# Kernel tuning notes

Measured on AMD Instinct MI355X. Metric: run time of the kernel, lower is better.

## Reference

```python
import jax, jax.numpy as jnp
import numpy as np

OBS_LEN, PRED_LEN, N, NUM_SEQ = 8, 12, 512, 8
H_ENC, H_DEC, EMB, NOISE_DIM = 8, 16, 16, 8


def setup_inputs() -> dict:
    key = jax.random.key(0)
    ks = jax.random.split(key, 32)
    def rn(i, shape, std=1.0):
        return jax.random.normal(ks[i], shape, jnp.float32) * std
    bounds = np.arange(NUM_SEQ + 1) * (N // NUM_SEQ)
    bih_t = jnp.zeros(4 * H_ENC, jnp.float32).at[H_ENC:2 * H_ENC].set(1.0)  # forget bias 1
    bih_p = jnp.zeros(4 * H_DEC, jnp.float32).at[H_DEC:2 * H_DEC].set(1.0)
    return {
        'traj_rel': rn(0, (OBS_LEN + PRED_LEN, N, 2)),
        'obs_traj_pos': rn(1, (OBS_LEN, N, 2), 5.0),
        'pred_traj_gt_pos': rn(2, (PRED_LEN, N, 2), 5.0),
        'h0': rn(3, (N, H_ENC)), 'c0': rn(4, (N, H_ENC)),
        'noise': rn(5, (NUM_SEQ, NOISE_DIM)),
        'W_enc': rn(6, (EMB, 2), 0.2), 'b_enc': jnp.zeros(EMB, jnp.float32),
        'W_dec': rn(7, (EMB, H_DEC + 2), 0.2), 'b_dec': jnp.zeros(EMB, jnp.float32),
        'Wih_t': rn(8, (4 * H_ENC, EMB), 0.1), 'Whh_t': rn(9, (4 * H_ENC, H_ENC), 0.001),
        'bih_t': bih_t, 'bhh_t': jnp.zeros(4 * H_ENC, jnp.float32),
        'Wih_p': rn(10, (4 * H_DEC, EMB), 0.1), 'Whh_p': rn(11, (4 * H_DEC, H_DEC), 0.001),
        'bih_p': bih_p, 'bhh_p': jnp.zeros(4 * H_DEC, jnp.float32),
        'W_out': rn(12, (2, H_DEC), 0.1), 'b_out': jnp.zeros(2, jnp.float32),
        'W_se': rn(13, (EMB, 2), 0.1), 'b_se': jnp.zeros(EMB, jnp.float32),
        'W_m1': rn(14, (64, EMB + H_DEC), 0.1), 'b_m1': jnp.zeros(64, jnp.float32),
        'W_m2': rn(15, (H_DEC, 64), 0.1), 'b_m2': jnp.zeros(H_DEC, jnp.float32),
        'W_att': rn(16, (1, H_DEC), 0.1), 'b_att': jnp.zeros(1, jnp.float32),
        'seq_start_end': jnp.asarray(np.stack([bounds[:-1], bounds[1:]], 1), jnp.int32),
        'nei_index': jax.random.randint(ks[17], (PRED_LEN, N, N), 0, 2, jnp.int32),
        'nei_num_index': jnp.full((N,), N // 2, jnp.int32),
    }


def _lstm_cell(x, h, c, Wih, Whh, bih, bhh):
    g = x @ Wih.T + bih + h @ Whh.T + bhh
    i, f, gg, o = jnp.split(g, 4, axis=-1)
    c2 = jax.nn.sigmoid(f) * c + jax.nn.sigmoid(i) * jnp.tanh(gg)
    return jax.nn.sigmoid(o) * jnp.tanh(c2), c2


def reference(traj_rel, obs_traj_pos, pred_traj_gt_pos, h0, c0, noise,
              W_enc, b_enc, W_dec, b_dec,
              Wih_t, Whh_t, bih_t, bhh_t,
              Wih_p, Whh_p, bih_p, bhh_p,
              W_out, b_out, W_se, b_se, W_m1, b_m1, W_m2, b_m2, W_att, b_att,
              seq_start_end, nei_index, nei_num_index):
    nb = traj_rel.shape[1]

    # ---- encoder: obs_len tiny LSTM steps over relative displacements ----
    def enc_step(carry, x_t):
        h, c = carry
        e = jax.nn.relu(x_t @ W_enc.T + b_enc)
        h, c = _lstm_cell(e, h, c, Wih_t, Whh_t, bih_t, bhh_t)
        return (h, c), None
    (h_enc, _), _ = jax.lax.scan(enc_step, (h0, c0), traj_rel[:OBS_LEN])

    # ---- add global per-scene noise (noise_mix_type == 'global') ----
    seq_ids = jnp.searchsorted(seq_start_end[:, 0], jnp.arange(nb), side='right') - 1
    dec_h = jnp.concatenate([h_enc, noise[seq_ids]], axis=1)  # [N, 16]

    def pool(pos, mask, h):
        # corr_index[i,j] = pos[i] - pos[j]
        corr = pos[:, None, :] - pos[None, :, :]                 # [N,N,2]
        r = corr @ W_se.T + b_se                                 # [N,N,EMB]
        hj = jnp.broadcast_to(h[None, :, :], (nb, nb, H_DEC))    # neighbor hidden
        m_in = jnp.concatenate([r, hj], axis=-1)                 # [N,N,EMB+H]
        h1 = jax.nn.relu(m_in @ W_m1.T + b_m1)                   # [N,N,64]
        pre = jax.nn.relu(h1 @ W_m2.T + b_m2)                    # [N,N,H]
        s = jnp.squeeze(pre @ W_att.T + b_att, -1)               # [N,N]
        s = jnp.where(mask, s, -1e9)
        w = jax.nn.softmax(s, axis=-1)
        ctx = jnp.einsum('ij,ijh->ih', w, pre)
        return jnp.where(mask.any(-1, keepdims=True), ctx, 0.0)

    # ---- decoder: pred_len steps with social pooling each step ----
    sg = jax.lax.stop_gradient
    init = (dec_h, jnp.zeros_like(dec_h), jnp.zeros_like(dec_h),
            jnp.zeros((nb, 2), dec_h.dtype), obs_traj_pos[-1])

    def dec_step(carry, nei_t):
        h, c, ctx, out, pos = carry
        inp_cat = jnp.concatenate([sg(ctx), sg(out)], axis=-1)   # [N, 18]
        e = jax.nn.relu(inp_cat @ W_dec.T + b_dec)
        h, c = _lstm_cell(e, h, c, Wih_p, Whh_p, bih_p, bhh_p)
        ctx = pool(pos, nei_t > 0, h)
        out = jnp.tanh((ctx + h) @ W_out.T + b_out) * 4.4
        pos = sg(pos + out)
        return (h, c, ctx, out, pos), out

    _, pred_traj_rel = jax.lax.scan(dec_step, init, nei_index)
    return pred_traj_rel  # [pred_len, N, 2]
```

## Files before the change

kernel.cpp:

```cpp
#include <hip/hip_runtime.h>
#include <math.h>

#define NPED 512
#define OBS 8
#define PRED 12
#define HE 8
#define HD 16
#define EMB 16
#define NZ 8
#define NSEQ 8

typedef const float* fp;
typedef float f4 __attribute__((ext_vector_type(4)));

__device__ __forceinline__ float frcp(float x){ return __builtin_amdgcn_rcpf(x); }
__device__ __forceinline__ float sigm(float x){ return frcp(1.0f + __expf(-x)); }
__device__ __forceinline__ float tanh_f(float x){ return 1.0f - 2.0f*frcp(__expf(2.0f*x) + 1.0f); }

#define WS_H    0
#define WS_C    (WS_H + NPED*HD)
#define WS_POS0 (WS_C + NPED*HD)
#define WS_POS1 (WS_POS0 + NPED*2)
#define WS_HB0  (WS_POS1 + NPED*2)
#define WS_HB1  (WS_HB0 + NPED*64)
#define WS_A0   (WS_HB1 + NPED*64)
#define WS_A1   (WS_A0 + 64)
#define WS_BB   (WS_A1 + 64)
#define WS_WM2T (WS_BB + 64)

__global__ __launch_bounds__(256) void init_kernel(
        fp traj, fp obs_pos, fp h0, fp c0, fp noise,
        fp Wenc, fp benc, fp Wih, fp Whh, fp bih, fp bhh,
        fp bdec, fp Wihp, fp Whhp, fp bihp, fp bhhp, fp Wm1,
        fp Wse, fp bse, fp bm1, fp Wm2,
        const int* sse, float* ws)
{
    __shared__ float s_wenc[32], s_benc[16], s_wihT[32*17], s_whhT[32*9], s_bT[32];
    __shared__ float s_wihP[64*17], s_whhP[64*17], s_wm1h[64*17], s_bP[64], s_e0[16];
    __shared__ float s_hc[16*16];
    int tid = threadIdx.x;

    if (blockIdx.x == 0) {
        if (tid < 64) {
            float a0 = 0.f, a1 = 0.f, bb = bm1[tid];
            for (int kk = 0; kk < 16; kk++) {
                float w = Wm1[tid*32 + kk];
                a0 += w*Wse[kk*2+0]; a1 += w*Wse[kk*2+1]; bb += w*bse[kk];
            }
            ws[WS_A0 + tid] = a0; ws[WS_A1 + tid] = a1; ws[WS_BB + tid] = bb;
        }
        for (int i = tid; i < 1024; i += 256) {
            int u = i >> 4, v = i & 15;
            ws[WS_WM2T + u*16 + v] = Wm2[v*64 + u];
        }
    }

    if (tid < 32) { s_wenc[tid] = Wenc[tid]; s_bT[tid] = bih[tid] + bhh[tid]; }
    if (tid < 16) { s_benc[tid] = benc[tid]; s_e0[tid] = fmaxf(bdec[tid], 0.f); }
    for (int i = tid; i < 512; i += 256) s_wihT[(i>>4)*17 + (i&15)] = Wih[i];
    { int i = tid; if (i < 256) s_whhT[(i>>3)*9 + (i&7)] = Whh[i]; }
    for (int i = tid; i < 1024; i += 256) {
        int r = i>>4, d = i&15;
        s_wihP[r*17+d] = Wihp[i];
        s_whhP[r*17+d] = Whhp[i];
        s_wm1h[r*17+d] = Wm1[r*32 + 16 + d];
    }
    if (tid < 64) s_bP[tid] = bihp[tid] + bhhp[tid];
    __syncthreads();

    int pid = tid >> 4, k16 = tid & 15;
    int n = blockIdx.x*16 + pid;

    if (k16 < 8) {
        int k = k16;
        float h = h0[n*HE+k], c = c0[n*HE+k];
        for (int t = 0; t < OBS; t++) {
            float x0 = traj[(t*NPED+n)*2+0];
            float x1 = traj[(t*NPED+n)*2+1];
            float g0 = s_bT[k], g1 = s_bT[8+k], g2 = s_bT[16+k], g3 = s_bT[24+k];
            #pragma unroll
            for (int d = 0; d < EMB; d++) {
                float e = fmaxf(s_wenc[d*2]*x0 + s_wenc[d*2+1]*x1 + s_benc[d], 0.f);
                g0 += s_wihT[(k)*17+d]*e;    g1 += s_wihT[(8+k)*17+d]*e;
                g2 += s_wihT[(16+k)*17+d]*e; g3 += s_wihT[(24+k)*17+d]*e;
            }
            #pragma unroll
            for (int d = 0; d < HE; d++) {
                float hv = __shfl(h, d, 8);
                g0 += s_whhT[(k)*9+d]*hv;    g1 += s_whhT[(8+k)*9+d]*hv;
                g2 += s_whhT[(16+k)*9+d]*hv; g3 += s_whhT[(24+k)*9+d]*hv;
            }
            c = sigm(g1)*c + sigm(g0)*tanh_f(g2);
            h = sigm(g3)*tanh_f(c);
        }
        int cnt = 0;
        #pragma unroll
        for (int s2 = 0; s2 < NSEQ; s2++) cnt += (sse[s2*2] <= n) ? 1 : 0;
        s_hc[pid*16 + k]     = h;
        s_hc[pid*16 + 8 + k] = noise[(cnt-1)*NZ + k];
    }
    __syncthreads();

    int k = k16;
    float h = s_hc[pid*16 + k];
    float g0 = s_bP[k], g1 = s_bP[16+k], g2 = s_bP[32+k], g3 = s_bP[48+k];
    #pragma unroll
    for (int d = 0; d < HD; d++) {
        float ev = s_e0[d];
        float hv = __shfl(h, d, 16);
        g0 += s_wihP[(k)*17+d]*ev    + s_whhP[(k)*17+d]*hv;
        g1 += s_wihP[(16+k)*17+d]*ev + s_whhP[(16+k)*17+d]*hv;
        g2 += s_wihP[(32+k)*17+d]*ev + s_whhP[(32+k)*17+d]*hv;
        g3 += s_wihP[(48+k)*17+d]*ev + s_whhP[(48+k)*17+d]*hv;
    }
    float c = sigm(g0)*tanh_f(g2);
    float hn = sigm(g3)*tanh_f(c);
    ws[WS_H + n*HD + k] = hn;
    ws[WS_C + n*HD + k] = c;

    float hb0=0.f, hb1=0.f, hb2=0.f, hb3=0.f;
    #pragma unroll
    for (int d = 0; d < HD; d++) {
        float hv = __shfl(hn, d, 16);
        hb0 += s_wm1h[(k)*17+d]*hv;    hb1 += s_wm1h[(16+k)*17+d]*hv;
        hb2 += s_wm1h[(32+k)*17+d]*hv; hb3 += s_wm1h[(48+k)*17+d]*hv;
    }
    float* hb = ws + WS_HB0 + n*64;
    hb[k] = hb0; hb[16+k] = hb1; hb[32+k] = hb2; hb[48+k] = hb3;
    if (k < 2) ws[WS_POS0 + n*2 + k] = obs_pos[((OBS-1)*NPED+n)*2 + k];
}

__global__ __launch_bounds__(512, 4) void pool_step_kernel(
        int t, int last, const int* nei,
        fp Wm1, fp bm2, fp Watt, fp batt,
        fp Wdec, fp bdec, fp Wihp, fp Whhp, fp bihp, fp bhhp, fp Wout, fp bout,
        float* ws, float* dout)
{
    __shared__ __align__(16) float s_A0[64], s_A1[64], s_BB[64];
    __shared__ __align__(16) float s_wm2t[1024];
    __shared__ __align__(16) float s_bm2[16], s_watt[16];
    __shared__ float s_batt;
    __shared__ float s_posx[NPED], s_posy[NPED];
    __shared__ int   s_list[NPED], s_cnt[8];
    __shared__ float s_mat[16*512];
    __shared__ float s_lred[8], s_mred[8], s_ctxacc[16], s_ctx[16];
    __shared__ float s_wdec[16*19], s_bdec[16], s_wout[32], s_bout[2];
    int tid = threadIdx.x;
    int i = blockIdx.x;

    int a = nei[((size_t)t*NPED + i)*NPED + tid] > 0;

    if (tid < 64) { s_A0[tid] = ws[WS_A0+tid]; s_A1[tid] = ws[WS_A1+tid]; s_BB[tid] = ws[WS_BB+tid]; }
    if (tid < 256) ((float4*)s_wm2t)[tid] = ((const float4*)(ws + WS_WM2T))[tid];
    if (tid < 16) { s_bm2[tid] = bm2[tid]; s_watt[tid] = Watt[tid]; }
    if (tid == 0) s_batt = batt[0];
    for (int q = tid; q < 288; q += 512) s_wdec[(q/18)*19 + (q%18)] = Wdec[q];
    if (tid < 16) s_bdec[tid] = bdec[tid];
    if (tid < 32) s_wout[tid] = Wout[tid];
    if (tid < 2)  s_bout[tid] = bout[tid];

    const float* posrd = ws + ((t & 1) ? WS_POS1 : WS_POS0);
    const float* hbrd  = ws + ((t & 1) ? WS_HB1  : WS_HB0 );
    float* poswr = ws + ((t & 1) ? WS_POS0 : WS_POS1);
    float* hbwr  = ws + ((t & 1) ? WS_HB0  : WS_HB1 );
    {
        const float2* p2 = (const float2*)posrd;
        float2 pp = p2[tid];
        s_posx[tid] = pp.x; s_posy[tid] = pp.y;
    }

    int w = tid >> 6, lane = tid & 63;
    unsigned long long below = (1ull << lane) - 1ull;

    unsigned long long mb = __ballot(a);
    if (lane == 0) s_cnt[w] = __popcll(mb);
    __syncthreads();
    int cnt = 0, base = 0;
    #pragma unroll
    for (int q = 0; q < 8; q++) {
        int cq = s_cnt[q];
        cnt += cq;
        if (q < w) base += cq;
    }
    if (a) s_list[base + __popcll(mb & below)] = tid;
    __syncthreads();

    float pix = s_posx[i], piy = s_posy[i];
    f4 pre4[4];
    #pragma unroll
    for (int q = 0; q < 4; q++) pre4[q] = (f4){0.f,0.f,0.f,0.f};
    float sc = -INFINITY;

    if (tid < cnt) {
        const f4* bm24 = (const f4*)s_bm2;
        pre4[0] = bm24[0]; pre4[1] = bm24[1]; pre4[2] = bm24[2]; pre4[3] = bm24[3];
        int j = s_list[tid];
        float cx = pix - s_posx[j], cy = piy - s_posy[j];
        const f4* HB4 = (const f4*)(hbrd + j*64);
        const f4* A04 = (const f4*)s_A0;
        const f4* A14 = (const f4*)s_A1;
        const f4* BB4 = (const f4*)s_BB;
        #pragma unroll
        for (int uq = 0; uq < 16; uq++) {
            f4 hb = HB4[uq];
            f4 h14 = A04[uq]*cx + A14[uq]*cy + (BB4[uq] + hb);
            h14 = __builtin_elementwise_max(h14, (f4){0.f,0.f,0.f,0.f});
            #define ACCU(s_, hval_) { \
                f4 hs = (f4){hval_, hval_, hval_, hval_}; \
                const f4* wr = (const f4*)(s_wm2t + (uq*4 + s_)*16); \
                pre4[0] = __builtin_elementwise_fma(wr[0], hs, pre4[0]); \
                pre4[1] = __builtin_elementwise_fma(wr[1], hs, pre4[1]); \
                pre4[2] = __builtin_elementwise_fma(wr[2], hs, pre4[2]); \
                pre4[3] = __builtin_elementwise_fma(wr[3], hs, pre4[3]); }
            ACCU(0, h14.x) ACCU(1, h14.y) ACCU(2, h14.z) ACCU(3, h14.w)
            #undef ACCU
        }
        f4 sacc = (f4){0.f,0.f,0.f,0.f};
        const f4* wa4 = (const f4*)s_watt;
        #pragma unroll
        for (int q = 0; q < 4; q++) {
            pre4[q] = __builtin_elementwise_max(pre4[q], (f4){0.f,0.f,0.f,0.f});
            sacc = __builtin_elementwise_fma(pre4[q], wa4[q], sacc);
        }
        sc = s_batt + (sacc.x + sacc.y) + (sacc.z + sacc.w);
    }

    float mloc = sc;
    #pragma unroll
    for (int off = 32; off >= 1; off >>= 1) mloc = fmaxf(mloc, __shfl_xor(mloc, off));
    if (lane == 0) s_mred[w] = mloc;
    __syncthreads();
    float M = s_mred[0];
    #pragma unroll
    for (int q = 1; q < 8; q++) M = fmaxf(M, s_mred[q]);

    float wexp = (tid < cnt) ? __expf(sc - M) : 0.f;
    float l = wexp;
    #pragma unroll
    for (int off = 32; off >= 1; off >>= 1) l += __shfl_xor(l, off);
    if (lane == 0) s_lred[w] = l;
    {
        const float* pa = (const float*)pre4;
        #pragma unroll
        for (int v = 0; v < 16; v++) s_mat[v*512 + tid] = wexp * pa[v];
    }
    __syncthreads();
    {
        int vv = tid >> 5, cc = tid & 31;
        float ssum = 0.f;
        #pragma unroll
        for (int e = 0; e < 16; e++) ssum += s_mat[vv*512 + cc + e*32];
        #pragma unroll
        for (int off = 16; off >= 1; off >>= 1) ssum += __shfl_xor(ssum, off, 32);
        if (cc == 0) s_ctxacc[vv] = ssum;
    }
    __syncthreads();
    if (tid < 16) {
        float cv = 0.f;
        if (cnt > 0) {
            float L = 0.f;
            #pragma unroll
            for (int q = 0; q < 8; q++) L += s_lred[q];
            cv = (L > 0.f) ? s_ctxacc[tid] / L : 0.f;
        }
        s_ctx[tid] = cv;
    }
    __syncthreads();

    if (tid < 64) {
        int r = tid;
        float h16 = 0.f, ctx16 = 0.f, cst = 0.f;
        if (r < 16) {
            h16   = ws[WS_H + i*HD + r];
            ctx16 = s_ctx[r];
            cst   = ws[WS_C + i*HD + r];
        }
        float ch = ctx16 + h16;
        float r0 = 0.f, r1 = 0.f;
        if (r < 16) { r0 = s_wout[r]*ch; r1 = s_wout[16+r]*ch; }
        #pragma unroll
        for (int off = 8; off >= 1; off >>= 1) {
            r0 += __shfl_xor(r0, off, 16);
            r1 += __shfl_xor(r1, off, 16);
        }
        float o0 = tanh_f(s_bout[0] + r0)*4.4f;
        float o1 = tanh_f(s_bout[1] + r1)*4.4f;
        if (r == 0) { dout[(t*NPED + i)*2 + 0] = o0; poswr[i*2+0] = pix + o0; }
        if (r == 1) { dout[(t*NPED + i)*2 + 1] = o1; poswr[i*2+1] = piy + o1; }

        if (!last) {
            float e = 0.f;
            if (r < 16) {
                e = s_bdec[r];
                #pragma unroll
                for (int d = 0; d < HD; d++) e += s_wdec[r*19 + d]*s_ctx[d];
                e += s_wdec[r*19+16]*o0 + s_wdec[r*19+17]*o1;
                e = fmaxf(e, 0.f);
            }
            const float4* wi4 = (const float4*)(Wihp + r*16);
            const float4* wh4 = (const float4*)(Whhp + r*16);
            float4 wi0 = wi4[0], wi1 = wi4[1], wi2 = wi4[2], wi3 = wi4[3];
            float4 wh0 = wh4[0], wh1 = wh4[1], wh2 = wh4[2], wh3 = wh4[3];
            float g = bihp[r] + bhhp[r];
            #define GD(wiv, whv, d0) { \
                g += wiv.x*__shfl(e, d0)   + whv.x*__shfl(h16, d0); \
                g += wiv.y*__shfl(e, d0+1) + whv.y*__shfl(h16, d0+1); \
                g += wiv.z*__shfl(e, d0+2) + whv.z*__shfl(h16, d0+2); \
                g += wiv.w*__shfl(e, d0+3) + whv.w*__shfl(h16, d0+3); }
            GD(wi0, wh0, 0) GD(wi1, wh1, 4) GD(wi2, wh2, 8) GD(wi3, wh3, 12)
            #undef GD
            float gi = __shfl(g, r & 15);
            float gf = __shfl(g, 16 + (r & 15));
            float gg = __shfl(g, 32 + (r & 15));
            float go = __shfl(g, 48 + (r & 15));
            float hn = 0.f;
            if (r < 16) {
                float cn = sigm(gf)*cst + sigm(gi)*tanh_f(gg);
                hn = sigm(go)*tanh_f(cn);
                ws[WS_H + i*HD + r] = hn;
                ws[WS_C + i*HD + r] = cn;
            }
            const float4* wm4 = (const float4*)(Wm1 + r*32 + 16);
            float4 m0 = wm4[0], m1 = wm4[1], m2 = wm4[2], m3 = wm4[3];
            float hb = 0.f;
            #define HBD(mv, d0) { \
                hb += mv.x*__shfl(hn, d0)   + mv.y*__shfl(hn, d0+1); \
                hb += mv.z*__shfl(hn, d0+2) + mv.w*__shfl(hn, d0+3); }
            HBD(m0, 0) HBD(m1, 4) HBD(m2, 8) HBD(m3, 12)
            #undef HBD
            hbwr[i*64 + r] = hb;
        }
    }
}

extern "C" void kernel_launch(void* const* d_in, const int* in_sizes, int n_in,
                              void* d_out, int out_size, void* d_ws, size_t ws_size,
                              hipStream_t stream)
{
    fp traj = (fp)d_in[0];
    fp obs  = (fp)d_in[1];
    fp h0   = (fp)d_in[3];
    fp c0   = (fp)d_in[4];
    fp noise= (fp)d_in[5];
    fp Wenc = (fp)d_in[6];  fp benc = (fp)d_in[7];
    fp Wdec = (fp)d_in[8];  fp bdec = (fp)d_in[9];
    fp Wiht = (fp)d_in[10]; fp Whht = (fp)d_in[11];
    fp biht = (fp)d_in[12]; fp bhht = (fp)d_in[13];
    fp Wihp = (fp)d_in[14]; fp Whhp = (fp)d_in[15];
    fp bihp = (fp)d_in[16]; fp bhhp = (fp)d_in[17];
    fp Wout = (fp)d_in[18]; fp bout = (fp)d_in[19];
    fp Wse  = (fp)d_in[20]; fp bse  = (fp)d_in[21];
    fp Wm1  = (fp)d_in[22]; fp bm1  = (fp)d_in[23];
    fp Wm2  = (fp)d_in[24]; fp bm2  = (fp)d_in[25];
    fp Watt = (fp)d_in[26]; fp batt = (fp)d_in[27];
    const int* sse = (const int*)d_in[28];
    const int* nei = (const int*)d_in[29];
    float* ws = (float*)d_ws;
    float* out = (float*)d_out;

    hipLaunchKernelGGL(init_kernel, dim3(32), dim3(256), 0, stream,
                       traj, obs, h0, c0, noise, Wenc, benc, Wiht, Whht, biht, bhht,
                       bdec, Wihp, Whhp, bihp, bhhp, Wm1, Wse, bse, bm1, Wm2, sse, ws);
    for (int t = 0; t < PRED; t++) {
        hipLaunchKernelGGL(pool_step_kernel, dim3(NPED), dim3(512), 0, stream,
                           t, (t == PRED-1) ? 1 : 0, nei,
                           Wm1, bm2, Watt, batt,
                           Wdec, bdec, Wihp, Whhp, bihp, bhhp, Wout, bout,
                           ws, out);
    }
}
```

Measured before the change: 169.9 us.

## Precompute hidden-state gate and output terms early in idle waves; prefetch HB rows

Waves 2 and 3 now compute the Whh·h gate contribution and the W_out·h output term at kernel start, before the pooling phase. This takes them off the serial tail that runs after the softmax/context reduction, and that tail now only handles the ctx- and e-dependent parts. The per-neighbor HB row is also loaded into registers in two batches of eight float4 up front, so the loads can overlap with compute. The cost is higher register pressure in the pool loop, which could lower occupancy under launch_bounds(512,4).

After: 171.9 us. Within noise of the previous version (+1.2%).

```diff
diff --git a/kernel.cpp b/kernel.cpp
--- a/kernel.cpp
+++ b/kernel.cpp
@@ -145,8 +145,10 @@
     __shared__ float s_mat[16*512];
     __shared__ float s_lred[8], s_mred[8], s_ctxacc[16], s_ctx[16];
     __shared__ float s_wdec[16*19], s_bdec[16], s_wout[32], s_bout[2];
+    __shared__ float s_gh[64], s_oh[2];
     int tid = threadIdx.x;
     int i = blockIdx.x;
+    int w = tid >> 6, lane = tid & 63;
 
     int a = nei[((size_t)t*NPED + i)*NPED + tid] > 0;
 
@@ -169,7 +171,29 @@
         s_posx[tid] = pp.x; s_posy[tid] = pp.y;
     }
 
-    int w = tid >> 6, lane = tid & 63;
+    if (w == 2) {
+        float hload = (lane < 16) ? ws[WS_H + i*HD + lane] : 0.f;
+        const float4* wh4 = (const float4*)(Whhp + lane*16);
+        float4 wh0 = wh4[0], wh1 = wh4[1], wh2 = wh4[2], wh3 = wh4[3];
+        float g = bihp[lane] + bhhp[lane];
+        #define GH(wv_, d0) { \
+            g += wv_.x*__shfl(hload, d0)   + wv_.y*__shfl(hload, d0+1); \
+            g += wv_.z*__shfl(hload, d0+2) + wv_.w*__shfl(hload, d0+3); }
+        GH(wh0, 0) GH(wh1, 4) GH(wh2, 8) GH(wh3, 12)
+        #undef GH
+        s_gh[lane] = g;
+    }
+    if (w == 3 && lane < 16) {
+        float hv = ws[WS_H + i*HD + lane];
+        float r0 = Wout[lane]*hv, r1 = Wout[16+lane]*hv;
+        #pragma unroll
+        for (int off = 8; off >= 1; off >>= 1) {
+            r0 += __shfl_xor(r0, off, 16);
+            r1 += __shfl_xor(r1, off, 16);
+        }
+        if (lane == 0) { s_oh[0] = r0; s_oh[1] = r1; }
+    }
+
     unsigned long long below = (1ull << lane) - 1ull;
 
     unsigned long long mb = __ballot(a);
@@ -197,24 +221,34 @@
         int j = s_list[tid];
         float cx = pix - s_posx[j], cy = piy - s_posy[j];
         const f4* HB4 = (const f4*)(hbrd + j*64);
+        f4 hbA[8], hbB[8];
+        #pragma unroll
+        for (int q = 0; q < 8; q++) hbA[q] = HB4[q];
+        #pragma unroll
+        for (int q = 0; q < 8; q++) hbB[q] = HB4[8+q];
         const f4* A04 = (const f4*)s_A0;
         const f4* A14 = (const f4*)s_A1;
         const f4* BB4 = (const f4*)s_BB;
-        #pragma unroll
-        for (int uq = 0; uq < 16; uq++) {
-            f4 hb = HB4[uq];
-            f4 h14 = A04[uq]*cx + A14[uq]*cy + (BB4[uq] + hb);
-            h14 = __builtin_elementwise_max(h14, (f4){0.f,0.f,0.f,0.f});
-            #define ACCU(s_, hval_) { \
-                f4 hs = (f4){hval_, hval_, hval_, hval_}; \
-                const f4* wr = (const f4*)(s_wm2t + (uq*4 + s_)*16); \
-                pre4[0] = __builtin_elementwise_fma(wr[0], hs, pre4[0]); \
-                pre4[1] = __builtin_elementwise_fma(wr[1], hs, pre4[1]); \
-                pre4[2] = __builtin_elementwise_fma(wr[2], hs, pre4[2]); \
-                pre4[3] = __builtin_elementwise_fma(wr[3], hs, pre4[3]); }
-            ACCU(0, h14.x) ACCU(1, h14.y) ACCU(2, h14.z) ACCU(3, h14.w)
-            #undef ACCU
-        }
+        #define BODY(uq, hbv) { \
+            f4 h14 = A04[uq]*cx + A14[uq]*cy + (BB4[uq] + hbv); \
+            h14 = __builtin_elementwise_max(h14, (f4){0.f,0.f,0.f,0.f}); \
+            { f4 hs = (f4){h14.x,h14.x,h14.x,h14.x}; const f4* wr = (const f4*)(s_wm2t + (uq*4+0)*16); \
+              pre4[0] = __builtin_elementwise_fma(wr[0], hs, pre4[0]); pre4[1] = __builtin_elementwise_fma(wr[1], hs, pre4[1]); \
+              pre4[2] = __builtin_elementwise_fma(wr[2], hs, pre4[2]); pre4[3] = __builtin_elementwise_fma(wr[3], hs, pre4[3]); } \
+            { f4 hs = (f4){h14.y,h14.y,h14.y,h14.y}; const f4* wr = (const f4*)(s_wm2t + (uq*4+1)*16); \
+              pre4[0] = __builtin_elementwise_fma(wr[0], hs, pre4[0]); pre4[1] = __builtin_elementwise_fma(wr[1], hs, pre4[1]); \
+              pre4[2] = __builtin_elementwise_fma(wr[2], hs, pre4[2]); pre4[3] = __builtin_elementwise_fma(wr[3], hs, pre4[3]); } \
+            { f4 hs = (f4){h14.z,h14.z,h14.z,h14.z}; const f4* wr = (const f4*)(s_wm2t + (uq*4+2)*16); \
+              pre4[0] = __builtin_elementwise_fma(wr[0], hs, pre4[0]); pre4[1] = __builtin_elementwise_fma(wr[1], hs, pre4[1]); \
+              pre4[2] = __builtin_elementwise_fma(wr[2], hs, pre4[2]); pre4[3] = __builtin_elementwise_fma(wr[3], hs, pre4[3]); } \
+            { f4 hs = (f4){h14.w,h14.w,h14.w,h14.w}; const f4* wr = (const f4*)(s_wm2t + (uq*4+3)*16); \
+              pre4[0] = __builtin_elementwise_fma(wr[0], hs, pre4[0]); pre4[1] = __builtin_elementwise_fma(wr[1], hs, pre4[1]); \
+              pre4[2] = __builtin_elementwise_fma(wr[2], hs, pre4[2]); pre4[3] = __builtin_elementwise_fma(wr[3], hs, pre4[3]); } }
+        #pragma unroll
+        for (int uq = 0; uq < 8; uq++) BODY(uq, hbA[uq])
+        #pragma unroll
+        for (int uq = 8; uq < 16; uq++) BODY(uq, hbB[uq-8])
+        #undef BODY
         f4 sacc = (f4){0.f,0.f,0.f,0.f};
         const f4* wa4 = (const f4*)s_watt;
         #pragma unroll
@@ -269,24 +303,18 @@
 
     if (tid < 64) {
         int r = tid;
-        float h16 = 0.f, ctx16 = 0.f, cst = 0.f;
-        if (r < 16) {
-            h16   = ws[WS_H + i*HD + r];
-            ctx16 = s_ctx[r];
-            cst   = ws[WS_C + i*HD + r];
-        }
-        float ch = ctx16 + h16;
+        float ctx16 = (r < 16) ? s_ctx[r] : 0.f;
         float r0 = 0.f, r1 = 0.f;
-        if (r < 16) { r0 = s_wout[r]*ch; r1 = s_wout[16+r]*ch; }
+        if (r < 16) { r0 = s_wout[r]*ctx16; r1 = s_wout[16+r]*ctx16; }
         #pragma unroll
         for (int off = 8; off >= 1; off >>= 1) {
             r0 += __shfl_xor(r0, off, 16);
             r1 += __shfl_xor(r1, off, 16);
         }
-        float o0 = tanh_f(s_bout[0] + r0)*4.4f;
-        float o1 = tanh_f(s_bout[1] + r1)*4.4f;
-        if (r == 0) { dout[(t*NPED + i)*2 + 0] = o0; poswr[i*2+0] = pix + o0; }
-        if (r == 1) { dout[(t*NPED + i)*2 + 1] = o1; poswr[i*2+1] = piy + o1; }
+        float o0 = tanh_f(s_bout[0] + r0 + s_oh[0])*4.4f;
+        float o1 = tanh_f(s_bout[1] + r1 + s_oh[1])*4.4f;
+        if (r == 0) { dout[(t*NPED + i)*2 + 0] = o0; poswr[i*2+0] = s_posx[i] + o0; }
+        if (r == 1) { dout[(t*NPED + i)*2 + 1] = o1; poswr[i*2+1] = s_posy[i] + o1; }
 
         if (!last) {
             float e = 0.f;
@@ -298,16 +326,12 @@
                 e = fmaxf(e, 0.f);
             }
             const float4* wi4 = (const float4*)(Wihp + r*16);
-            const float4* wh4 = (const float4*)(Whhp + r*16);
             float4 wi0 = wi4[0], wi1 = wi4[1], wi2 = wi4[2], wi3 = wi4[3];
-            float4 wh0 = wh4[0], wh1 = wh4[1], wh2 = wh4[2], wh3 = wh4[3];
-            float g = bihp[r] + bhhp[r];
-            #define GD(wiv, whv, d0) { \
-                g += wiv.x*__shfl(e, d0)   + whv.x*__shfl(h16, d0); \
-                g += wiv.y*__shfl(e, d0+1) + whv.y*__shfl(h16, d0+1); \
-                g += wiv.z*__shfl(e, d0+2) + whv.z*__shfl(h16, d0+2); \
-                g += wiv.w*__shfl(e, d0+3) + whv.w*__shfl(h16, d0+3); }
-            GD(wi0, wh0, 0) GD(wi1, wh1, 4) GD(wi2, wh2, 8) GD(wi3, wh3, 12)
+            float g = s_gh[r];
+            #define GD(wiv, d0) { \
+                g += wiv.x*__shfl(e, d0)   + wiv.y*__shfl(e, d0+1); \
+                g += wiv.z*__shfl(e, d0+2) + wiv.w*__shfl(e, d0+3); }
+            GD(wi0, 0) GD(wi1, 4) GD(wi2, 8) GD(wi3, 12)
             #undef GD
             float gi = __shfl(g, r & 15);
             float gf = __shfl(g, 16 + (r & 15));
@@ -315,6 +339,7 @@
             float go = __shfl(g, 48 + (r & 15));
             float hn = 0.f;
             if (r < 16) {
+                float cst = ws[WS_C + i*HD + r];
                 float cn = sigm(gf)*cst + sigm(gi)*tanh_f(gg);
                 hn = sigm(go)*tanh_f(cn);
                 ws[WS_H + i*HD + r] = hn;
```

## Precompute next step's neighbor list in current step kernel via global workspace

Applied to the files above, without the earlier changes.

Each pool step now reads the neighbor mask for step t+1 and writes a compacted neighbor list and count to double-buffered global workspace. The next step loads its list directly instead of doing ballot compaction and an extra barrier on the critical path. This moves the mask load and compaction off the dependency chain between the load and the MLP work, at the cost of extra global writes of up to 512x512 ints per step and more workspace.

New measurement: 177.9 us. 4.7% more time.

```diff
diff --git a/kernel.cpp b/kernel.cpp
--- a/kernel.cpp
+++ b/kernel.cpp
@@ -27,6 +27,10 @@
 #define WS_A1   (WS_A0 + 64)
 #define WS_BB   (WS_A1 + 64)
 #define WS_WM2T (WS_BB + 64)
+#define WS_CNT0 (WS_WM2T + 1024)
+#define WS_CNT1 (WS_CNT0 + NPED)
+#define WS_LIST0 (WS_CNT1 + NPED)
+#define WS_LIST1 (WS_LIST0 + NPED*NPED)
 
 __global__ __launch_bounds__(256) void init_kernel(
         fp traj, fp obs_pos, fp h0, fp c0, fp noise,
@@ -141,14 +145,24 @@
     __shared__ __align__(16) float s_bm2[16], s_watt[16];
     __shared__ float s_batt;
     __shared__ float s_posx[NPED], s_posy[NPED];
-    __shared__ int   s_list[NPED], s_cnt[8];
+    __shared__ int   s_list[NPED], s_cnt[8], s_cnt2[8];
     __shared__ float s_mat[16*512];
     __shared__ float s_lred[8], s_mred[8], s_ctxacc[16], s_ctx[16];
     __shared__ float s_wdec[16*19], s_bdec[16], s_wout[32], s_bout[2];
     int tid = threadIdx.x;
     int i = blockIdx.x;
-
-    int a = nei[((size_t)t*NPED + i)*NPED + tid] > 0;
+    int w = tid >> 6, lane = tid & 63;
+    unsigned long long below = (1ull << lane) - 1ull;
+    int* wsi = (int*)ws;
+
+    int a0 = 0, a_next = 0;
+    if (t == 0) a0 = nei[(size_t)i*NPED + tid] > 0;
+    if (t < PRED-1) a_next = nei[((size_t)(t+1)*NPED + i)*NPED + tid] > 0;
+    int cnt = 0, jmine = 0;
+    if (t > 0) {
+        cnt   = wsi[((t & 1) ? WS_CNT1 : WS_CNT0) + i];
+        jmine = wsi[((t & 1) ? WS_LIST1 : WS_LIST0) + i*NPED + tid] & (NPED-1);
+    }
 
     if (tid < 64) { s_A0[tid] = ws[WS_A0+tid]; s_A1[tid] = ws[WS_A1+tid]; s_BB[tid] = ws[WS_BB+tid]; }
     if (tid < 256) ((float4*)s_wm2t)[tid] = ((const float4*)(ws + WS_WM2T))[tid];
@@ -169,21 +183,23 @@
         s_posx[tid] = pp.x; s_posy[tid] = pp.y;
     }
 
-    int w = tid >> 6, lane = tid & 63;
-    unsigned long long below = (1ull << lane) - 1ull;
-
-    unsigned long long mb = __ballot(a);
-    if (lane == 0) s_cnt[w] = __popcll(mb);
-    __syncthreads();
-    int cnt = 0, base = 0;
-    #pragma unroll
-    for (int q = 0; q < 8; q++) {
-        int cq = s_cnt[q];
-        cnt += cq;
-        if (q < w) base += cq;
-    }
-    if (a) s_list[base + __popcll(mb & below)] = tid;
-    __syncthreads();
+    if (t == 0) {
+        unsigned long long mb = __ballot(a0);
+        if (lane == 0) s_cnt[w] = __popcll(mb);
+        __syncthreads();
+        int base = 0; cnt = 0;
+        #pragma unroll
+        for (int q = 0; q < 8; q++) {
+            int cq = s_cnt[q];
+            cnt += cq;
+            if (q < w) base += cq;
+        }
+        if (a0) s_list[base + __popcll(mb & below)] = tid;
+        __syncthreads();
+        if (tid < cnt) jmine = s_list[tid];
+    } else {
+        __syncthreads();
+    }
 
     float pix = s_posx[i], piy = s_posy[i];
     f4 pre4[4];
@@ -194,7 +210,7 @@
     if (tid < cnt) {
         const f4* bm24 = (const f4*)s_bm2;
         pre4[0] = bm24[0]; pre4[1] = bm24[1]; pre4[2] = bm24[2]; pre4[3] = bm24[3];
-        int j = s_list[tid];
+        int j = jmine;
         float cx = pix - s_posx[j], cy = piy - s_posy[j];
         const f4* HB4 = (const f4*)(hbrd + j*64);
         const f4* A04 = (const f4*)s_A0;
@@ -229,10 +245,25 @@
     #pragma unroll
     for (int off = 32; off >= 1; off >>= 1) mloc = fmaxf(mloc, __shfl_xor(mloc, off));
     if (lane == 0) s_mred[w] = mloc;
+    unsigned long long mbn = __ballot(a_next);
+    if (t < PRED-1 && lane == 0) s_cnt2[w] = __popcll(mbn);
     __syncthreads();
     float M = s_mred[0];
     #pragma unroll
     for (int q = 1; q < 8; q++) M = fmaxf(M, s_mred[q]);
+
+    if (t < PRED-1) {
+        int cum = 0, basen = 0;
+        #pragma unroll
+        for (int q = 0; q < 8; q++) {
+            int cq = s_cnt2[q];
+            cum += cq;
+            if (q < w) basen += cq;
+        }
+        int lbuf = (((t+1) & 1) ? WS_LIST1 : WS_LIST0);
+        if (a_next) wsi[lbuf + i*NPED + basen + __popcll(mbn & below)] = tid;
+        if (tid == 0) wsi[((((t+1) & 1)) ? WS_CNT1 : WS_CNT0) + i] = cum;
+    }
 
     float wexp = (tid < cnt) ? __expf(sc - M) : 0.f;
     float l = wexp;
```
